# Performance work log

Hardware: AMD Instinct MI355X
Metric: run time of the kernel (lower is better)

## Reference

```python
import jax, jax.numpy as jnp
import numpy as np

B, L, H, F, D = 8, 2048, 1024, 256, 3  # batch, seq, d_model, adapter bottleneck, non-news domains
EPS = 1e-6  # annotated-transformer LayerNorm eps


def setup_inputs() -> dict:
    key = jax.random.key(0)
    ks = jax.random.split(key, 6)
    s1 = 1.0 / np.sqrt(H)
    s2 = 1.0 / np.sqrt(F)
    return {
        "x": jax.random.normal(ks[0], (B, L, H), jnp.float32),
        # per-domain LayerNorm params (SublayerConnection.norm)
        "ln_g": jnp.ones((D, H), jnp.float32),
        "ln_b": jnp.zeros((D, H), jnp.float32),
        # per-domain adapter FFN: Linear(H->F), ReLU, Linear(F->H)
        "W1": (jax.random.normal(ks[1], (D, F, H), jnp.float32) * s1),
        "b1": jnp.zeros((D, F), jnp.float32),
        "W2": (jax.random.normal(ks[2], (D, H, F), jnp.float32) * s2),
        "b2": jnp.zeros((D, H), jnp.float32),
        # per-domain gate Linear(2H -> 1), split into the x-half (gu) and adapter-half (gv)
        "gu": (jax.random.normal(ks[3], (D, H), jnp.float32) * s1),
        "gv": (jax.random.normal(ks[4], (D, H), jnp.float32) * s1),
        "gb": jnp.zeros((D,), jnp.float32),
    }


def reference(x, ln_g, ln_b, W1, b1, W2, b2, gu, gv, gb):
    # mix_output=True, used_domain_list=['news','book','bible','iwslt'],
    # target_domain='book' (in list -> no extra pass), dropout=eval (identity).
    mu = jnp.mean(x, axis=-1, keepdims=True)
    sd = jnp.std(x, axis=-1, keepdims=True, ddof=1)  # torch .std default (unbiased)
    xn = (x - mu) / (sd + EPS)                        # shared normalization stats
    # per-domain LayerNorm affine -> [D,B,L,H]
    h = xn[None] * ln_g[:, None, None, :] + ln_b[:, None, None, :]
    # adapter FFN (wo_residual_forward): Linear -> ReLU -> Linear
    mid = jax.nn.relu(jnp.einsum('dblh,dfh->dblf', h, W1) + b1[:, None, None, :])
    a = jnp.einsum('dblf,dhf->dblh', mid, W2) + b2[:, None, None, :]  # [D,B,L,H]
    # gate = sigmoid(Linear([x; a])) with W_gate split as [gu | gv]
    gate = jax.nn.sigmoid(
        jnp.einsum('blh,dh->dbl', x, gu)
        + jnp.einsum('dblh,dh->dbl', a, gv)
        + gb[:, None, None]
    )  # [D,B,L]
    # stacked sum includes 'news' contribution (= x), then outer residual +x:
    return 2.0 * x + jnp.sum(gate[..., None] * a, axis=0)
```

## Files before the change

### kernel.cpp

```cpp
#include <hip/hip_runtime.h>
#include <cstdint>

#define T_TOK 16384
#define H 1024
#define F 256
#define D 3
#define DF 768

typedef unsigned short u16;
typedef __attribute__((ext_vector_type(8))) short short8;
typedef __attribute__((ext_vector_type(4))) float floatx4;

__device__ __forceinline__ u16 f2bf(float f) {
  unsigned u = __float_as_uint(f);
  u += 0x7fff + ((u >> 16) & 1);
  return (u16)(u >> 16);
}
__device__ __forceinline__ float bf2f(u16 s) {
  return __uint_as_float(((unsigned)s) << 16);
}

__device__ __forceinline__ void gload_lds16(const void* g, void* l) {
  __builtin_amdgcn_global_load_lds(
      reinterpret_cast<const __attribute__((address_space(1))) void*>(
          reinterpret_cast<uintptr_t>(g)),
      reinterpret_cast<__attribute__((address_space(3))) void*>(
          reinterpret_cast<uintptr_t>(l)),
      16, 0, 0);
}

__device__ __forceinline__ float block_reduce_256(float v, float* red, int tid) {
  #pragma unroll
  for (int o = 32; o > 0; o >>= 1) v += __shfl_xor(v, o);
  __syncthreads();
  if ((tid & 63) == 0) red[tid >> 6] = v;
  __syncthreads();
  return red[0] + red[1] + red[2] + red[3];
}


__global__ __launch_bounds__(256)
void prep_elem(const float* __restrict__ W1, const float* __restrict__ lng,
               u16* __restrict__ W1p, const float* __restrict__ W2,
               u16* __restrict__ W2r)
{
  int idx = blockIdx.x * 256 + threadIdx.x;
  int stride = gridDim.x * 256;
  for (int i = idx; i < D * F * H; i += stride) {
    int h = i & (H - 1);
    int d = i / (F * H);
    W1p[i] = f2bf(W1[i] * lng[d * H + h]);
  }
  for (int i = idx; i < H * DF; i += stride) {
    int k = i % DF;
    int hh = i / DF;
    int d = k >> 8;
    int f = k & (F - 1);
    W2r[i] = f2bf(W2[((size_t)d * H + hh) * F + f]);
  }
}

__global__ __launch_bounds__(256)
void prep_dots(const float* __restrict__ W1, const float* __restrict__ lnb,
               const float* __restrict__ b1, const float* __restrict__ W2,
               const float* __restrict__ gv, const float* __restrict__ b2,
               const float* __restrict__ gb, float* __restrict__ b1p,
               float* __restrict__ wg, float* __restrict__ cg)
{
  __shared__ float red[4];
  int d = blockIdx.x >> 8;
  int f = blockIdx.x & 255;
  int tid = threadIdx.x;
  float s1 = 0.f, s2 = 0.f, s3 = 0.f;
  for (int h = tid; h < H; h += 256) {
    float w1v = W1[((size_t)d * F + f) * H + h];
    float gvv = gv[d * H + h];
    s1 += lnb[d * H + h] * w1v;
    s2 += W2[((size_t)d * H + h) * F + f] * gvv;
    if (f == 0) s3 += b2[d * H + h] * gvv;
  }
  float S1 = block_reduce_256(s1, red, tid);
  float S2 = block_reduce_256(s2, red, tid);
  if (tid == 0) {
    b1p[d * F + f] = b1[d * F + f] + S1;
    wg[d * F + f] = S2;
  }
  if (f == 0) {
    float S3 = block_reduce_256(s3, red, tid);
    if (tid == 0) cg[d] = gb[d] + S3;
  }
}

__global__ __launch_bounds__(256)
void ln_xu_kernel(const float* __restrict__ x, const float* __restrict__ gu,
                  u16* __restrict__ xn, float* __restrict__ xu)
{
  int t = blockIdx.x;
  int tid = threadIdx.x;
  const float4 xv = *reinterpret_cast<const float4*>(x + (size_t)t * H + tid * 4);
  const float4 g0 = *reinterpret_cast<const float4*>(gu + tid * 4);
  const float4 g1 = *reinterpret_cast<const float4*>(gu + H + tid * 4);
  const float4 g2 = *reinterpret_cast<const float4*>(gu + 2 * H + tid * 4);
  float s  = xv.x + xv.y + xv.z + xv.w;
  float sq = xv.x * xv.x + xv.y * xv.y + xv.z * xv.z + xv.w * xv.w;
  float d0 = xv.x * g0.x + xv.y * g0.y + xv.z * g0.z + xv.w * g0.w;
  float d1 = xv.x * g1.x + xv.y * g1.y + xv.z * g1.z + xv.w * g1.w;
  float d2 = xv.x * g2.x + xv.y * g2.y + xv.z * g2.z + xv.w * g2.w;
  #pragma unroll
  for (int o = 32; o > 0; o >>= 1) {
    s  += __shfl_xor(s, o);  sq += __shfl_xor(sq, o);
    d0 += __shfl_xor(d0, o); d1 += __shfl_xor(d1, o); d2 += __shfl_xor(d2, o);
  }
  __shared__ float red[4][5];
  int w = tid >> 6;
  if ((tid & 63) == 0) {
    red[w][0] = s; red[w][1] = sq; red[w][2] = d0; red[w][3] = d1; red[w][4] = d2;
  }
  __syncthreads();
  float S  = red[0][0] + red[1][0] + red[2][0] + red[3][0];
  float SQ = red[0][1] + red[1][1] + red[2][1] + red[3][1];
  float mu = S * (1.0f / H);
  float var = (SQ - (float)H * mu * mu) * (1.0f / (H - 1));
  float rs = 1.0f / (sqrtf(fmaxf(var, 0.0f)) + 1e-6f);
  ushort4 o4;
  o4.x = f2bf((xv.x - mu) * rs);
  o4.y = f2bf((xv.y - mu) * rs);
  o4.z = f2bf((xv.z - mu) * rs);
  o4.w = f2bf((xv.w - mu) * rs);
  *reinterpret_cast<ushort4*>(xn + (size_t)t * H + tid * 4) = o4;
  if (tid == 0) {
    xu[t]             = red[0][2] + red[1][2] + red[2][2] + red[3][2];
    xu[T_TOK + t]     = red[0][3] + red[1][3] + red[2][3] + red[3][3];
    xu[2 * T_TOK + t] = red[0][4] + red[1][4] + red[2][4] + red[3][4];
  }
}

template <int K, int NLD, int EPI>
__global__ __launch_bounds__(512, 4)
void gemm2p(const u16* __restrict__ A, const u16* __restrict__ Bm,
            const float* __restrict__ p0,
            const float* __restrict__ p1,
            const float* __restrict__ p2,
            const float* __restrict__ p3,
            u16* __restrict__ o16,
            float* __restrict__ o32,
            int nBx)
{
  constexpr int NT = K / 32;
  constexpr int BUF = 12288;
  extern __shared__ u16 LD[];

  const int tid = threadIdx.x, lane = tid & 63, w = tid >> 6;
  const int wm = w >> 2, wn = w & 3, lr = lane & 15, sl = lane >> 4;

  const int bid = blockIdx.x;
  const int xcd = bid & 7, idx = bid >> 3;
  const int by = xcd * 16 + idx / nBx;
  const int bx = idx % nBx;
  const int m0 = by * 128, n0 = bx * 256;

  const u16* Asrc = A + (size_t)m0 * K;
  const u16* Bsrc = Bm + (size_t)n0 * K;

  const int sc = (tid & 3) ^ ((tid >> 3) & 3);
  const int srcA  = (tid >> 2) * K + sc * 8;
  const int srcB1 = srcA + 128 * K;
  const int dstA  = w * 512;
  const int dstB0 = 4096 + w * 512;
  const int dstB1 = 8192 + w * 512;

  const int key = (lr >> 1) & 3;
  const int rsl = (sl ^ key) << 3;
  const int aoff = (wm * 64 + lr) * 32 + rsl;
  const int boff = 4096 + (wn * 64 + lr) * 32 + rsl;

  floatx4 acc[4][4] = {};
  short8 a[4], b[4];

#define STG(BP, T_) do { int kb_ = (T_) * 32; \
    gload_lds16(Asrc + srcA + kb_, (BP) + dstA); \
    gload_lds16(Bsrc + srcA + kb_, (BP) + dstB0); \
    gload_lds16(Bsrc + srcB1 + kb_, (BP) + dstB1); \
  } while (0)
#define LDAB(BP) do { \
    const u16* sa_ = (BP) + aoff; const u16* sb_ = (BP) + boff; \
    _Pragma("unroll") for (int i_ = 0; i_ < 4; ++i_) { \
      a[i_] = *reinterpret_cast<const short8*>(sa_ + i_ * 512); \
      b[i_] = *reinterpret_cast<const short8*>(sb_ + i_ * 512); } } while (0)
#define MMX() do { \
    _Pragma("unroll") for (int mf_ = 0; mf_ < 4; ++mf_) \
      _Pragma("unroll") for (int nf_ = 0; nf_ < 4; ++nf_) \
        acc[mf_][nf_] = __builtin_amdgcn_mfma_f32_16x16x32_bf16( \
            a[mf_], b[nf_], acc[mf_][nf_], 0, 0, 0); } while (0)

  STG(LD, 0);
  __syncthreads();

  #pragma unroll 1
  for (int t = 0; t < NT - 1; ++t) {
    u16* cur = LD + (t & 1) * BUF;
    u16* nxt = LD + ((t + 1) & 1) * BUF;
    STG(nxt, t + 1);
    LDAB(cur);
    MMX();
    __syncthreads();
  }
  LDAB(LD + ((NT - 1) & 1) * BUF);
  MMX();
  __syncthreads();

  if constexpr (EPI == 1) {
    float b1v[4], wgv[4];
    #pragma unroll
    for (int nf = 0; nf < 4; ++nf) {
      int col = n0 + wn * 64 + nf * 16 + lr;
      b1v[nf] = p0[col];
      wgv[nf] = p1[col];
    }
    float* red = (float*)LD;
    #pragma unroll
    for (int mf = 0; mf < 4; ++mf)
      #pragma unroll
      for (int i2 = 0; i2 < 4; ++i2) {
        float p = 0.f;
        #pragma unroll
        for (int nf = 0; nf < 4; ++nf)
          p += fmaxf(acc[mf][nf][i2] + b1v[nf], 0.f) * wgv[nf];
        p += __shfl_xor(p, 1); p += __shfl_xor(p, 2);
        p += __shfl_xor(p, 4); p += __shfl_xor(p, 8);
        if (lr == 0) red[wn * 128 + wm * 64 + mf * 16 + sl * 4 + i2] = p;
      }
    __syncthreads();
    const int d = bx;
    const float cgv = p3[d];
    float gv_[4][4];
    #pragma unroll
    for (int mf = 0; mf < 4; ++mf)
      #pragma unroll
      for (int i2 = 0; i2 < 4; ++i2) {
        int rl = wm * 64 + mf * 16 + sl * 4 + i2;
        int r = m0 + rl;
        float logit = red[rl] + red[128 + rl] + red[256 + rl] + red[384 + rl]
                    + p2[(size_t)d * T_TOK + r] + cgv;
        float g = 1.f / (1.f + expf(-logit));
        gv_[mf][i2] = g;
        if (lr == 0 && wn == 0) o32[(size_t)d * T_TOK + r] = g;
      }
    __syncthreads();
    #pragma unroll
    for (int mf = 0; mf < 4; ++mf)
      #pragma unroll
      for (int i2 = 0; i2 < 4; ++i2) {
        int rl = wm * 64 + mf * 16 + sl * 4 + i2;
        #pragma unroll
        for (int nf = 0; nf < 4; ++nf) {
          int cl = wn * 64 + nf * 16 + lr;
          float v = fmaxf(acc[mf][nf][i2] + b1v[nf], 0.f);
          LD[rl * 264 + cl] = f2bf(v * gv_[mf][i2]);
        }
      }
    __syncthreads();
    #pragma unroll
    for (int ps = 0; ps < 8; ++ps) {
      int q = ps * 512 + tid;
      int row = q >> 5, ch = q & 31;
      short8 v = *reinterpret_cast<const short8*>(LD + row * 264 + ch * 8);
      *reinterpret_cast<short8*>(&o16[(size_t)(m0 + row) * NLD + n0 + ch * 8]) = v;
    }
  } else {
    float b2v[3][4];
    #pragma unroll
    for (int dd = 0; dd < 3; ++dd)
      #pragma unroll
      for (int nf = 0; nf < 4; ++nf)
        b2v[dd][nf] = p2[dd * H + n0 + wn * 64 + nf * 16 + lr];
    #pragma unroll
    for (int mf = 0; mf < 4; ++mf)
      #pragma unroll
      for (int i2 = 0; i2 < 4; ++i2) {
        int r = m0 + wm * 64 + mf * 16 + sl * 4 + i2;
        float g0 = p1[r], g1 = p1[T_TOK + r], g2 = p1[2 * T_TOK + r];
        const float* xrow = p0 + (size_t)r * H;
        float* orow = o32 + (size_t)r * NLD;
        #pragma unroll
        for (int nf = 0; nf < 4; ++nf) {
          int col = n0 + wn * 64 + nf * 16 + lr;
          orow[col] = acc[mf][nf][i2] + 2.f * xrow[col]
                    + g0 * b2v[0][nf] + g1 * b2v[1][nf] + g2 * b2v[2][nf];
        }
      }
  }
#undef STG
#undef LDAB
#undef MMX
}


extern "C" void kernel_launch(void* const* d_in, const int* in_sizes, int n_in,
                              void* d_out, int out_size, void* d_ws, size_t ws_size,
                              hipStream_t stream) {
  const float* x   = (const float*)d_in[0];
  const float* lng = (const float*)d_in[1];
  const float* lnb = (const float*)d_in[2];
  const float* W1  = (const float*)d_in[3];
  const float* b1  = (const float*)d_in[4];
  const float* W2  = (const float*)d_in[5];
  const float* b2  = (const float*)d_in[6];
  const float* gu  = (const float*)d_in[7];
  const float* gv  = (const float*)d_in[8];
  const float* gb  = (const float*)d_in[9];
  float* out = (float*)d_out;

  char* ws = (char*)d_ws;
  u16* xn   = (u16*)ws;  ws += (size_t)T_TOK * H * 2;
  u16* mid  = (u16*)ws;  ws += (size_t)T_TOK * DF * 2;
  u16* W1p  = (u16*)ws;  ws += (size_t)DF * H * 2;
  u16* W2r  = (u16*)ws;  ws += (size_t)H * DF * 2;
  float* b1p  = (float*)ws;  ws += DF * 4;
  float* wg   = (float*)ws;  ws += DF * 4;
  float* cg   = (float*)ws;  ws += 256;
  float* xu   = (float*)ws;  ws += (size_t)D * T_TOK * 4;
  float* gate = (float*)ws;  ws += (size_t)D * T_TOK * 4;
  (void)ws_size; (void)in_sizes; (void)n_in; (void)out_size;

  hipFuncSetAttribute(reinterpret_cast<const void*>(&gemm2p<1024, DF, 1>),
                      hipFuncAttributeMaxDynamicSharedMemorySize, 67584);
  hipFuncSetAttribute(reinterpret_cast<const void*>(&gemm2p<768, H, 2>),
                      hipFuncAttributeMaxDynamicSharedMemorySize, 49152);

  prep_elem<<<3072, 256, 0, stream>>>(W1, lng, W1p, W2, W2r);
  prep_dots<<<DF, 256, 0, stream>>>(W1, lnb, b1, W2, gv, b2, gb, b1p, wg, cg);
  ln_xu_kernel<<<T_TOK, 256, 0, stream>>>(x, gu, xn, xu);
  gemm2p<1024, DF, 1><<<128 * 3, 512, 67584, stream>>>(
      xn, W1p, b1p, wg, xu, cg, mid, gate, 3);
  gemm2p<768, H, 2><<<128 * 4, 512, 49152, stream>>>(
      mid, W2r, x, gate, b2, nullptr, nullptr, out, 4);
}
```

Baseline: 127.3 us.

## Use 4-wave GEMM blocks with 64x128 per-wave tiles

```diff
diff --git a/kernel.cpp b/kernel.cpp
--- a/kernel.cpp
+++ b/kernel.cpp
@@ -136,7 +136,7 @@
 }
 
 template <int K, int NLD, int EPI>
-__global__ __launch_bounds__(512, 4)
+__global__ __launch_bounds__(256, 3)
 void gemm2p(const u16* __restrict__ A, const u16* __restrict__ Bm,
             const float* __restrict__ p0,
             const float* __restrict__ p1,
@@ -151,7 +151,7 @@
   extern __shared__ u16 LD[];
 
   const int tid = threadIdx.x, lane = tid & 63, w = tid >> 6;
-  const int wm = w >> 2, wn = w & 3, lr = lane & 15, sl = lane >> 4;
+  const int wm = w >> 1, wn = w & 1, lr = lane & 15, sl = lane >> 4;
 
   const int bid = blockIdx.x;
   const int xcd = bid & 7, idx = bid >> 3;
@@ -163,33 +163,35 @@
   const u16* Bsrc = Bm + (size_t)n0 * K;
 
   const int sc = (tid & 3) ^ ((tid >> 3) & 3);
-  const int srcA  = (tid >> 2) * K + sc * 8;
-  const int srcB1 = srcA + 128 * K;
-  const int dstA  = w * 512;
-  const int dstB0 = 4096 + w * 512;
-  const int dstB1 = 8192 + w * 512;
+  const int gsrc = (tid >> 2) * K + sc * 8;
+  const int dstA = w * 512;
+  const int dstB = 4096 + w * 512;
 
   const int key = (lr >> 1) & 3;
   const int rsl = (sl ^ key) << 3;
   const int aoff = (wm * 64 + lr) * 32 + rsl;
-  const int boff = 4096 + (wn * 64 + lr) * 32 + rsl;
-
-  floatx4 acc[4][4] = {};
-  short8 a[4], b[4];
+  const int boff = 4096 + (wn * 128 + lr) * 32 + rsl;
+
+  floatx4 acc[4][8] = {};
+  short8 a[4], b[8];
 
 #define STG(BP, T_) do { int kb_ = (T_) * 32; \
-    gload_lds16(Asrc + srcA + kb_, (BP) + dstA); \
-    gload_lds16(Bsrc + srcA + kb_, (BP) + dstB0); \
-    gload_lds16(Bsrc + srcB1 + kb_, (BP) + dstB1); \
+    gload_lds16(Asrc + gsrc + kb_,           (BP) + dstA); \
+    gload_lds16(Asrc + gsrc + 64 * K + kb_,  (BP) + dstA + 2048); \
+    gload_lds16(Bsrc + gsrc + kb_,           (BP) + dstB); \
+    gload_lds16(Bsrc + gsrc + 64 * K + kb_,  (BP) + dstB + 2048); \
+    gload_lds16(Bsrc + gsrc + 128 * K + kb_, (BP) + dstB + 4096); \
+    gload_lds16(Bsrc + gsrc + 192 * K + kb_, (BP) + dstB + 6144); \
   } while (0)
 #define LDAB(BP) do { \
     const u16* sa_ = (BP) + aoff; const u16* sb_ = (BP) + boff; \
-    _Pragma("unroll") for (int i_ = 0; i_ < 4; ++i_) { \
+    _Pragma("unroll") for (int i_ = 0; i_ < 4; ++i_) \
       a[i_] = *reinterpret_cast<const short8*>(sa_ + i_ * 512); \
-      b[i_] = *reinterpret_cast<const short8*>(sb_ + i_ * 512); } } while (0)
+    _Pragma("unroll") for (int j_ = 0; j_ < 8; ++j_) \
+      b[j_] = *reinterpret_cast<const short8*>(sb_ + j_ * 512); } while (0)
 #define MMX() do { \
     _Pragma("unroll") for (int mf_ = 0; mf_ < 4; ++mf_) \
-      _Pragma("unroll") for (int nf_ = 0; nf_ < 4; ++nf_) \
+      _Pragma("unroll") for (int nf_ = 0; nf_ < 8; ++nf_) \
         acc[mf_][nf_] = __builtin_amdgcn_mfma_f32_16x16x32_bf16( \
             a[mf_], b[nf_], acc[mf_][nf_], 0, 0, 0); } while (0)
 
@@ -210,10 +212,10 @@
   __syncthreads();
 
   if constexpr (EPI == 1) {
-    float b1v[4], wgv[4];
-    #pragma unroll
-    for (int nf = 0; nf < 4; ++nf) {
-      int col = n0 + wn * 64 + nf * 16 + lr;
+    float b1v[8], wgv[8];
+    #pragma unroll
+    for (int nf = 0; nf < 8; ++nf) {
+      int col = n0 + wn * 128 + nf * 16 + lr;
       b1v[nf] = p0[col];
       wgv[nf] = p1[col];
     }
@@ -224,7 +226,7 @@
       for (int i2 = 0; i2 < 4; ++i2) {
         float p = 0.f;
         #pragma unroll
-        for (int nf = 0; nf < 4; ++nf)
+        for (int nf = 0; nf < 8; ++nf)
           p += fmaxf(acc[mf][nf][i2] + b1v[nf], 0.f) * wgv[nf];
         p += __shfl_xor(p, 1); p += __shfl_xor(p, 2);
         p += __shfl_xor(p, 4); p += __shfl_xor(p, 8);
@@ -240,40 +242,48 @@
       for (int i2 = 0; i2 < 4; ++i2) {
         int rl = wm * 64 + mf * 16 + sl * 4 + i2;
         int r = m0 + rl;
-        float logit = red[rl] + red[128 + rl] + red[256 + rl] + red[384 + rl]
+        float logit = red[rl] + red[128 + rl]
                     + p2[(size_t)d * T_TOK + r] + cgv;
         float g = 1.f / (1.f + expf(-logit));
         gv_[mf][i2] = g;
         if (lr == 0 && wn == 0) o32[(size_t)d * T_TOK + r] = g;
       }
     __syncthreads();
-    #pragma unroll
-    for (int mf = 0; mf < 4; ++mf)
-      #pragma unroll
-      for (int i2 = 0; i2 < 4; ++i2) {
-        int rl = wm * 64 + mf * 16 + sl * 4 + i2;
+    u16* tile = LD + 512;
+    #pragma unroll
+    for (int ph = 0; ph < 2; ++ph) {
+      if (wm == ph) {
         #pragma unroll
-        for (int nf = 0; nf < 4; ++nf) {
-          int cl = wn * 64 + nf * 16 + lr;
-          float v = fmaxf(acc[mf][nf][i2] + b1v[nf], 0.f);
-          LD[rl * 264 + cl] = f2bf(v * gv_[mf][i2]);
-        }
-      }
-    __syncthreads();
-    #pragma unroll
-    for (int ps = 0; ps < 8; ++ps) {
-      int q = ps * 512 + tid;
-      int row = q >> 5, ch = q & 31;
-      short8 v = *reinterpret_cast<const short8*>(LD + row * 264 + ch * 8);
-      *reinterpret_cast<short8*>(&o16[(size_t)(m0 + row) * NLD + n0 + ch * 8]) = v;
+        for (int mf = 0; mf < 4; ++mf)
+          #pragma unroll
+          for (int i2 = 0; i2 < 4; ++i2) {
+            int rl = mf * 16 + sl * 4 + i2;
+            #pragma unroll
+            for (int nf = 0; nf < 8; ++nf) {
+              int cl = wn * 128 + nf * 16 + lr;
+              float v = fmaxf(acc[mf][nf][i2] + b1v[nf], 0.f);
+              tile[rl * 264 + cl] = f2bf(v * gv_[mf][i2]);
+            }
+          }
+      }
+      __syncthreads();
+      #pragma unroll
+      for (int it = 0; it < 8; ++it) {
+        int q = it * 256 + tid;
+        int row = q >> 5, ch = q & 31;
+        short8 v = *reinterpret_cast<const short8*>(tile + row * 264 + ch * 8);
+        *reinterpret_cast<short8*>(
+            &o16[(size_t)(m0 + ph * 64 + row) * NLD + n0 + ch * 8]) = v;
+      }
+      __syncthreads();
     }
   } else {
-    float b2v[3][4];
+    float b2v[3][8];
     #pragma unroll
     for (int dd = 0; dd < 3; ++dd)
       #pragma unroll
-      for (int nf = 0; nf < 4; ++nf)
-        b2v[dd][nf] = p2[dd * H + n0 + wn * 64 + nf * 16 + lr];
+      for (int nf = 0; nf < 8; ++nf)
+        b2v[dd][nf] = p2[dd * H + n0 + wn * 128 + nf * 16 + lr];
     #pragma unroll
     for (int mf = 0; mf < 4; ++mf)
       #pragma unroll
@@ -283,8 +293,8 @@
         const float* xrow = p0 + (size_t)r * H;
         float* orow = o32 + (size_t)r * NLD;
         #pragma unroll
-        for (int nf = 0; nf < 4; ++nf) {
-          int col = n0 + wn * 64 + nf * 16 + lr;
+        for (int nf = 0; nf < 8; ++nf) {
+          int col = n0 + wn * 128 + nf * 16 + lr;
           orow[col] = acc[mf][nf][i2] + 2.f * xrow[col]
                     + g0 * b2v[0][nf] + g1 * b2v[1][nf] + g2 * b2v[2][nf];
         }
@@ -324,15 +334,15 @@
   (void)ws_size; (void)in_sizes; (void)n_in; (void)out_size;
 
   hipFuncSetAttribute(reinterpret_cast<const void*>(&gemm2p<1024, DF, 1>),
-                      hipFuncAttributeMaxDynamicSharedMemorySize, 67584);
+                      hipFuncAttributeMaxDynamicSharedMemorySize, 49152);
   hipFuncSetAttribute(reinterpret_cast<const void*>(&gemm2p<768, H, 2>),
                       hipFuncAttributeMaxDynamicSharedMemorySize, 49152);
 
   prep_elem<<<3072, 256, 0, stream>>>(W1, lng, W1p, W2, W2r);
   prep_dots<<<DF, 256, 0, stream>>>(W1, lnb, b1, W2, gv, b2, gb, b1p, wg, cg);
   ln_xu_kernel<<<T_TOK, 256, 0, stream>>>(x, gu, xn, xu);
-  gemm2p<1024, DF, 1><<<128 * 3, 512, 67584, stream>>>(
+  gemm2p<1024, DF, 1><<<128 * 3, 256, 49152, stream>>>(
       xn, W1p, b1p, wg, xu, cg, mid, gate, 3);
-  gemm2p<768, H, 2><<<128 * 4, 512, 49152, stream>>>(
+  gemm2p<768, H, 2><<<128 * 4, 256, 49152, stream>>>(
       mid, W2r, x, gate, b2, nullptr, nullptr, out, 4);
 }
```

Result: slower. 174.1 us (+36.8%).
